# Optimization experiments

Hardware: AMD Instinct MI355X
Metric: run time of the kernel (lower is better)

## Reference

```python
import jax, jax.numpy as jnp
import numpy as np
from jax import lax

L1_DECAY = 1e-06


def _maxpool2(x):
    # NCHW 2x2 max pool, stride 2
    return lax.reduce_window(x, -jnp.inf, lax.max, (1, 1, 2, 2), (1, 1, 2, 2), 'VALID')


def _cnn(x, w1, b1, w2, b2, wo, bo):
    # x: [N,128,128] -> [N,64], z-score normalized over batch dim
    x = x[:, None]  # [N,1,128,128]
    dn = ('NCHW', 'OIHW', 'NCHW')
    x = lax.conv_general_dilated(x, w1, (1, 1), 'SAME', dimension_numbers=dn) + b1[None, :, None, None]
    x = _maxpool2(jax.nn.relu(x))  # [N,4,64,64]
    x = lax.conv_general_dilated(x, w2, (1, 1), 'SAME', dimension_numbers=dn) + b2[None, :, None, None]
    x = _maxpool2(jax.nn.relu(x))  # [N,8,32,32]
    x = x.reshape(x.shape[0], -1)  # [N,8192] (C,H,W order, as torch .view)
    x = x @ wo.T + bo  # [N,64]
    mean = x.mean(axis=0)
    std = x.std(axis=0, ddof=1)  # torch unbiased std
    return (x - mean) / std


def _interact(item, nbr):
    # item: [N,64]; nbr: [N,H,K,64]. dot-attention over K per node/hop.
    scores = jnp.einsum('nhkd,nd->nhk', nbr, item)
    attn = jax.nn.softmax(scores, axis=-1)
    return jnp.einsum('nhk,nhkd->nhd', attn, nbr)  # [N,H,64]


def setup_inputs() -> dict:
    key = jax.random.key(0)
    ks = jax.random.split(key, 16)
    B = 4096
    inp = {}
    inp['data'] = jax.random.randint(ks[0], (B, 3), 0, 76)
    inp['cell_nbr'] = jax.random.randint(ks[1], (76, 2, 128), 0, 15970)
    inp['drug_nbr'] = jax.random.randint(ks[2], (764, 2, 128), 0, 15970)
    inp['protein_table'] = jax.random.normal(ks[3], (15970, 64), jnp.float32)
    inp['cell_emb_pre'] = jax.random.normal(ks[4], (76, 128, 128), jnp.float32)
    inp['drug_emb_pre'] = jax.random.normal(ks[5], (764, 128, 128), jnp.float32)
    inp['conv1_w'] = 0.05 * jax.random.normal(ks[6], (4, 1, 3, 3), jnp.float32)
    inp['conv1_b'] = 0.05 * jax.random.normal(ks[7], (4,), jnp.float32)
    inp['conv2_w'] = 0.05 * jax.random.normal(ks[8], (8, 4, 3, 3), jnp.float32)
    inp['conv2_b'] = 0.05 * jax.random.normal(ks[9], (8,), jnp.float32)
    inp['out_w'] = 0.05 * jax.random.normal(ks[10], (64, 8192), jnp.float32)
    inp['out_b'] = 0.05 * jax.random.normal(ks[11], (64,), jnp.float32)
    inp['agg_w'] = 0.05 * jax.random.normal(ks[12], (64, 128), jnp.float32)
    inp['agg_b'] = 0.05 * jax.random.normal(ks[13], (64,), jnp.float32)
    inp['comb_w'] = 0.05 * jax.random.normal(ks[14], (64, 128), jnp.float32)
    return inp


def reference(data, cell_nbr, drug_nbr, protein_table, cell_emb_pre, drug_emb_pre,
              conv1_w, conv1_b, conv2_w, conv2_b, out_w, out_b, agg_w, agg_b, comb_w):
    cells, drug1, drug2 = data[:, 0], data[:, 1], data[:, 2]
    B = data.shape[0]

    # per-node neighbor embedding gather: [num, n_hop, K, 64]
    cell_nbr_emb = protein_table[cell_nbr]
    drug_nbr_emb = protein_table[drug_nbr]

    # CNN item embeddings from precomputed images
    cell_item = _cnn(cell_emb_pre, conv1_w, conv1_b, conv2_w, conv2_b, out_w, out_b)  # [76,64]
    drug_item = _cnn(drug_emb_pre, conv1_w, conv1_b, conv2_w, conv2_b, out_w, out_b)  # [764,64]

    # gather -> attend -> weighted sum, then concat hops and aggregate
    cell_i = _interact(cell_item, cell_nbr_emb).reshape(cell_item.shape[0], -1)  # [76,128]
    drug_i = _interact(drug_item, drug_nbr_emb).reshape(drug_item.shape[0], -1)  # [764,128]
    cell_emb = cell_i @ agg_w.T + agg_b  # [76,64]
    drug_emb = drug_i @ agg_w.T + agg_b  # [764,64]

    # batch gather, keep singleton dim 1 to match torch stacking of [1,64]
    ce = cell_emb[cells][:, None, :]   # [B,1,64]
    d1e = drug_emb[drug1][:, None, :]
    d2e = drug_emb[drug2][:, None, :]

    # therapy: transformation_matrix
    combined = jnp.concatenate([d1e, d2e], axis=2) @ comb_w.T  # [B,1,64]
    therapy = (combined * ce).sum(axis=2)  # [B,1]
    toxic = (d1e * d2e).sum(axis=2)        # [B,1]
    score = therapy - toxic

    # emb loss (faithful to source: neighbor lists are indexed on the BATCH dim by hop)
    cnl = cell_nbr_emb[cells]   # [B,2,128,64]
    dnl1 = drug_nbr_emb[drug1]
    dnl2 = drug_nbr_emb[drug2]
    sq = lambda t: jnp.sum(t * t)
    item_reg = (sq(ce) + sq(d1e) + sq(d2e)) / 2
    node_reg = jnp.float32(0.0)
    for hop in range(2):
        node_reg = node_reg + (sq(cnl[hop]) + sq(dnl1[hop]) + sq(dnl2[hop])) / 2
    emb_loss = L1_DECAY * (item_reg + node_reg) / B
    return score, emb_loss
```

## Files before the change

kernel.cpp:

```cpp
#include <hip/hip_runtime.h>
#include <hip/hip_bf16.h>
#include <math.h>

#define N_CELL 76
#define N_DRUG 764
#define N_ITEM 840
#define BATCH  4096

#define POOL2H_B 55050240u
#define POOL2L_B 68812800u
#define WHI_B    0u
#define WLO_B    1048576u
#define XFC_B    2097152u
#define ITEM_B   2312192u
#define EMB_B    2527232u
#define V_B      2742272u
#define LOSS_B   2781184u

typedef short bh8 __attribute__((ext_vector_type(8)));
typedef short bh4 __attribute__((ext_vector_type(4)));
typedef float f32x4 __attribute__((ext_vector_type(4)));

static __device__ inline unsigned short f2bf(float f) {
  union { float f; unsigned u; } v; v.f = f;
  unsigned r = v.u + 0x7FFFu + ((v.u >> 16) & 1u);
  return (unsigned short)(r >> 16);
}
static __device__ inline float bf2f(unsigned short h) {
  union { unsigned u; float f; } v; v.u = ((unsigned)h) << 16;
  return v.f;
}
static __device__ inline unsigned short f2bf_lo(float f, unsigned short h) {
  union { float f; unsigned u; } a; a.f = f - bf2f(h);
  return (unsigned short)(a.u >> 16);
}

__global__ __launch_bounds__(256) void k_conv1(
    const float* __restrict__ cell_pre, const float* __restrict__ drug_pre,
    const float* __restrict__ w1, const float* __restrict__ b1,
    float* __restrict__ pool1) {
  __shared__ float img[66 * 128];
  int half = blockIdx.x, n = blockIdx.y;
  int tid = threadIdx.x;
  int cy0 = half * 64;
  const float* src = (n < N_CELL) ? (cell_pre + (size_t)n * 16384)
                                  : (drug_pre + (size_t)(n - N_CELL) * 16384);
  for (int i = tid; i < 66 * 32; i += 256) {
    int r = i >> 5, c = i & 31;
    int iy = cy0 - 1 + r;
    float4 v = make_float4(0.f, 0.f, 0.f, 0.f);
    if (iy >= 0 && iy < 128) v = ((const float4*)src)[iy * 32 + c];
    ((float4*)img)[i] = v;
  }
  float wv[4][9], bb[4];
#pragma unroll
  for (int c = 0; c < 4; ++c) {
    bb[c] = b1[c];
#pragma unroll
    for (int j = 0; j < 9; ++j) wv[c][j] = w1[c * 9 + j];
  }
  __syncthreads();
  int t = tid & 31;
  int g = tid >> 5;
  const float4* img4 = (const float4*)img;
#pragma unroll 1
  for (int rpi = 0; rpi < 4; ++rpi) {
    int rp = g + 8 * rpi;
    int ly = 2 * rp;
    float4 rowv[4]; float lo[4], hi[4];
#pragma unroll
    for (int rr = 0; rr < 4; ++rr) {
      rowv[rr] = img4[(ly + rr) * 32 + t];
      float l = __shfl_up(rowv[rr].w, 1);
      float h = __shfl_down(rowv[rr].x, 1);
      lo[rr] = (t == 0) ? 0.f : l;
      hi[rr] = (t == 31) ? 0.f : h;
    }
    float a[2][4][4];
#pragma unroll
    for (int orow = 0; orow < 2; ++orow)
#pragma unroll
      for (int oc = 0; oc < 4; ++oc)
#pragma unroll
        for (int c = 0; c < 4; ++c) a[orow][oc][c] = bb[oc];
#pragma unroll
    for (int orow = 0; orow < 2; ++orow) {
#pragma unroll
      for (int kr = 0; kr < 3; ++kr) {
        int rr = orow + kr;
        float in[6] = {lo[rr], rowv[rr].x, rowv[rr].y, rowv[rr].z, rowv[rr].w, hi[rr]};
#pragma unroll
        for (int ks = 0; ks < 3; ++ks)
#pragma unroll
          for (int oc = 0; oc < 4; ++oc) {
            float w = wv[oc][kr * 3 + ks];
#pragma unroll
            for (int c = 0; c < 4; ++c) a[orow][oc][c] += in[c + ks] * w;
          }
      }
    }
#pragma unroll
    for (int pc = 0; pc < 2; ++pc) {
      float4 res;
      float* resf = (float*)&res;
#pragma unroll
      for (int oc = 0; oc < 4; ++oc) {
        float m = fmaxf(fmaxf(a[0][oc][2 * pc], a[0][oc][2 * pc + 1]),
                        fmaxf(a[1][oc][2 * pc], a[1][oc][2 * pc + 1]));
        resf[oc] = fmaxf(m, 0.f);
      }
      int py = half * 32 + rp, px = 2 * t + pc;
      ((float4*)pool1)[((size_t)n * 64 + py) * 64 + px] = res;
    }
  }
}

__global__ __launch_bounds__(256) void k_conv2(
    const float* __restrict__ pool1, const float* __restrict__ w2,
    const float* __restrict__ b2, unsigned short* __restrict__ pool2h,
    unsigned short* __restrict__ pool2l) {
  __shared__ unsigned short lh[34 * 66 * 4];
  __shared__ unsigned short ll[34 * 66 * 4];
  int half = blockIdx.x, n = blockIdx.y;
  int tid = threadIdx.x;
  int cy0 = half * 32;
  const float4* src = (const float4*)(pool1 + (size_t)n * 16384);
  for (int i = tid; i < 34 * 64; i += 256) {
    int r = i >> 6, c = i & 63;
    int iy = cy0 - 1 + r;
    float4 v = make_float4(0.f, 0.f, 0.f, 0.f);
    if (iy >= 0 && iy < 64) v = src[iy * 64 + c];
    ushort4 h, l;
    h.x = f2bf(v.x); l.x = f2bf_lo(v.x, h.x);
    h.y = f2bf(v.y); l.y = f2bf_lo(v.y, h.y);
    h.z = f2bf(v.z); l.z = f2bf_lo(v.z, h.z);
    h.w = f2bf(v.w); l.w = f2bf_lo(v.w, h.w);
    ((ushort4*)lh)[r * 66 + c + 1] = h;
    ((ushort4*)ll)[r * 66 + c + 1] = l;
  }
  if (tid < 68) {
    int r = tid >> 1, c = (tid & 1) ? 65 : 0;
    ushort4 z = make_ushort4(0, 0, 0, 0);
    ((ushort4*)lh)[r * 66 + c] = z;
    ((ushort4*)ll)[r * 66 + c] = z;
  }
  int wv_ = tid >> 6;
  int lane = tid & 63;
  int ml = lane & 15, q = lane >> 4;
  int oc_b = ml & 7, yv = ml >> 3;
  bh8 Bh[2], Bl[2];
#pragma unroll
  for (int ch = 0; ch < 2; ++ch) {
#pragma unroll
    for (int j = 0; j < 8; ++j) {
      int kg = ch * 32 + q * 8 + j;
      float v = 0.f;
      if (kg < 48) {
        int r = kg / 12, rem = kg - r * 12;
        int ks = rem >> 2, ic = rem & 3;
        int kr = r - yv;
        if (kr >= 0 && kr <= 2) v = w2[(oc_b * 4 + ic) * 9 + kr * 3 + ks];
      } else if (kg == 48) {
        v = b2[oc_b];
      }
      unsigned short h = f2bf(v);
      Bh[ch][j] = (short)h;
      Bl[ch][j] = (short)f2bf_lo(v, h);
    }
  }
  int c0 = 2 * q, c1 = 2 * q + 1;
  int c2 = 8 + 2 * q, c3 = 9 + 2 * q;
  if (c2 > 11) { c2 = 8; c3 = 9; }
  int r0 = (c0 * 86) >> 8, s0 = c0 - 3 * r0;
  int r1 = (c1 * 86) >> 8, s1 = c1 - 3 * r1;
  int r2 = (c2 * 86) >> 8, s2 = c2 - 3 * r2;
  int r3 = (c3 * 86) >> 8, s3 = c3 - 3 * r3;
  int x0 = (wv_ & 3) << 4;
  int off0 = r0 * 66 + x0 + ml + s0;
  int off1 = r1 * 66 + x0 + ml + s1;
  int off2 = r2 * 66 + x0 + ml + s2;
  int off3 = r3 * 66 + x0 + ml + s3;
  __syncthreads();
  const bh4* lh4 = (const bh4*)lh;
  const bh4* ll4 = (const bh4*)ll;
  union BH8U { bh8 v; struct { bh4 lo, hi; } s; };
#pragma unroll 1
  for (int rp = 0; rp < 16; ++rp) {
    int base = 2 * rp * 66;
    BH8U ah0, al0, ah1, al1;
    ah0.s.lo = lh4[base + off0]; ah0.s.hi = lh4[base + off1];
    al0.s.lo = ll4[base + off0]; al0.s.hi = ll4[base + off1];
    if (q < 2) {
      ah1.s.lo = lh4[base + off2]; ah1.s.hi = lh4[base + off3];
      al1.s.lo = ll4[base + off2]; al1.s.hi = ll4[base + off3];
    } else {
#pragma unroll
      for (int j = 0; j < 8; ++j) { ah1.v[j] = 0; al1.v[j] = 0; }
      if (q == 2) ah1.v[0] = (short)0x3F80;
    }
    f32x4 accA = {0.f, 0.f, 0.f, 0.f}, accB = accA;
    accA = __builtin_amdgcn_mfma_f32_16x16x32_bf16(ah0.v, Bh[0], accA, 0, 0, 0);
    accA = __builtin_amdgcn_mfma_f32_16x16x32_bf16(ah0.v, Bl[0], accA, 0, 0, 0);
    accA = __builtin_amdgcn_mfma_f32_16x16x32_bf16(al0.v, Bh[0], accA, 0, 0, 0);
    accB = __builtin_amdgcn_mfma_f32_16x16x32_bf16(ah1.v, Bh[1], accB, 0, 0, 0);
    accB = __builtin_amdgcn_mfma_f32_16x16x32_bf16(ah1.v, Bl[1], accB, 0, 0, 0);
    accB = __builtin_amdgcn_mfma_f32_16x16x32_bf16(al1.v, Bh[1], accB, 0, 0, 0);
    float d0 = accA[0] + accB[0], d1 = accA[1] + accB[1];
    float d2 = accA[2] + accB[2], d3 = accA[3] + accB[3];
    float m0 = fmaxf(d0, d1), m1 = fmaxf(d2, d3);
    float o0 = __shfl_xor(m0, 8), o1 = __shfl_xor(m1, 8);
    m0 = fmaxf(fmaxf(m0, o0), 0.f);
    m1 = fmaxf(fmaxf(m1, o1), 0.f);
    if (yv == 0) {
      unsigned short h0 = f2bf(m0), h1 = f2bf(m1);
      unsigned short l0 = f2bf(m0 - bf2f(h0)), l1 = f2bf(m1 - bf2f(h1));
      int PR = half * 16 + rp;
      unsigned ui = (unsigned)n * 4096u + (unsigned)oc_b * 512u +
                    (unsigned)PR * 16u + (unsigned)(x0 >> 2) + (unsigned)q;
      ((unsigned*)pool2h)[ui] = (unsigned)h0 | ((unsigned)h1 << 16);
      ((unsigned*)pool2l)[ui] = (unsigned)l0 | ((unsigned)l1 << 16);
    }
  }
}

__global__ __launch_bounds__(256) void k_cast(
    const float* __restrict__ out_w, unsigned short* __restrict__ whi,
    unsigned short* __restrict__ wlo, float* __restrict__ xfc,
    float* __restrict__ loss) {
  int gid = blockIdx.x * 256 + threadIdx.x;
  if (gid == 0) *loss = 0.f;
  float4 v = ((const float4*)out_w)[gid];
  ushort4 h, l;
  h.x = f2bf(v.x); l.x = f2bf(v.x - bf2f(h.x));
  h.y = f2bf(v.y); l.y = f2bf(v.y - bf2f(h.y));
  h.z = f2bf(v.z); l.z = f2bf(v.z - bf2f(h.z));
  h.w = f2bf(v.w); l.w = f2bf(v.w - bf2f(h.w));
  ((ushort4*)whi)[gid] = h;
  ((ushort4*)wlo)[gid] = l;
  if (gid < N_ITEM * 64) xfc[gid] = 0.f;
}

__global__ __launch_bounds__(64) void k_fc(
    const unsigned short* __restrict__ pool2h, const unsigned short* __restrict__ pool2l,
    const unsigned short* __restrict__ whi, const unsigned short* __restrict__ wlo,
    float* __restrict__ xfc) {
  int mt = blockIdx.x, kc = blockIdx.y;
  int lane = threadIdx.x;
  int ml = lane & 15, q = lane >> 4;
  int row = mt * 16 + ml; if (row > N_ITEM - 1) row = N_ITEM - 1;
  size_t k0 = (size_t)kc * 256 + q * 8;
  const bh8* Ah = (const bh8*)(pool2h + (size_t)row * 8192 + k0);
  const bh8* Al = (const bh8*)(pool2l + (size_t)row * 8192 + k0);
  const bh8* Bh[4], * Bl[4];
#pragma unroll
  for (int nb = 0; nb < 4; ++nb) {
    Bh[nb] = (const bh8*)(whi + (size_t)(nb * 16 + ml) * 8192 + k0);
    Bl[nb] = (const bh8*)(wlo + (size_t)(nb * 16 + ml) * 8192 + k0);
  }
  f32x4 acc[4];
#pragma unroll
  for (int nb = 0; nb < 4; ++nb) acc[nb] = (f32x4){0.f, 0.f, 0.f, 0.f};
#pragma unroll
  for (int st = 0; st < 8; ++st) {
    bh8 ah = Ah[st * 4], al = Al[st * 4];
#pragma unroll
    for (int nb = 0; nb < 4; ++nb) {
      bh8 bhv = Bh[nb][st * 4], blv = Bl[nb][st * 4];
      acc[nb] = __builtin_amdgcn_mfma_f32_16x16x32_bf16(ah, bhv, acc[nb], 0, 0, 0);
      acc[nb] = __builtin_amdgcn_mfma_f32_16x16x32_bf16(ah, blv, acc[nb], 0, 0, 0);
      acc[nb] = __builtin_amdgcn_mfma_f32_16x16x32_bf16(al, bhv, acc[nb], 0, 0, 0);
    }
  }
#pragma unroll
  for (int r = 0; r < 4; ++r) {
    int mr = mt * 16 + q * 4 + r;
    if (mr < N_ITEM) {
      float* dst = xfc + (size_t)mr * 64 + ml;
#pragma unroll
      for (int nb = 0; nb < 4; ++nb) atomicAdd(dst + nb * 16, acc[nb][r]);
    }
  }
}

__global__ __launch_bounds__(256) void k_norm(
    const float* __restrict__ xfc, float* __restrict__ item) {
  __shared__ float red[256];
  int grp = blockIdx.x >> 6;
  int o = blockIdx.x & 63;
  int base = grp ? N_CELL : 0;
  int N = grp ? N_DRUG : N_CELL;
  int tid = threadIdx.x;
  float s = 0.f;
  for (int i = tid; i < N; i += 256) s += xfc[(size_t)(base + i) * 64 + o];
  red[tid] = s; __syncthreads();
  for (int w = 128; w > 0; w >>= 1) { if (tid < w) red[tid] += red[tid + w]; __syncthreads(); }
  float mean = red[0] / (float)N;
  __syncthreads();
  float sq = 0.f;
  for (int i = tid; i < N; i += 256) {
    float d = xfc[(size_t)(base + i) * 64 + o] - mean;
    sq += d * d;
  }
  red[tid] = sq; __syncthreads();
  for (int w = 128; w > 0; w >>= 1) { if (tid < w) red[tid] += red[tid + w]; __syncthreads(); }
  float inv_std = 1.f / sqrtf(red[0] / (float)(N - 1));
  for (int i = tid; i < N; i += 256)
    item[(size_t)(base + i) * 64 + o] = (xfc[(size_t)(base + i) * 64 + o] - mean) * inv_std;
}

__global__ __launch_bounds__(256) void k_interact(
    const int* __restrict__ cell_nbr, const int* __restrict__ drug_nbr,
    const float* __restrict__ protein, const float* __restrict__ item,
    const float* __restrict__ agg_w, const float* __restrict__ agg_b,
    float* __restrict__ emb) {
  __shared__ float pb[128 * 65];
  __shared__ float item_s[64];
  __shared__ float sc[128];
  __shared__ float hop_out[128];
  __shared__ float red[256];
  int n = blockIdx.x;
  int tid = threadIdx.x;
  const int* nbr = (n < N_CELL) ? (cell_nbr + (size_t)n * 256)
                                : (drug_nbr + (size_t)(n - N_CELL) * 256);
  if (tid < 64) item_s[tid] = item[(size_t)n * 64 + tid];
  __syncthreads();
  for (int h = 0; h < 2; ++h) {
    for (int e = tid; e < 8192; e += 256) {
      int k = e >> 6, d = e & 63;
      int idx = nbr[h * 128 + k];
      pb[k * 65 + d] = protein[(size_t)idx * 64 + d];
    }
    __syncthreads();
    {
      int k = tid >> 1, halfd = tid & 1;
      int d0 = halfd * 32;
      float p = 0.f;
#pragma unroll
      for (int d = 0; d < 32; ++d) p += item_s[d0 + d] * pb[k * 65 + d0 + d];
      p += __shfl_xor(p, 1);
      if (halfd == 0) sc[k] = p;
    }
    __syncthreads();
    if (tid < 64) {
      float a = sc[tid], b = sc[tid + 64];
      float m = fmaxf(a, b);
#pragma unroll
      for (int off = 32; off > 0; off >>= 1) m = fmaxf(m, __shfl_xor(m, off));
      float e0 = __expf(a - m), e1 = __expf(b - m);
      float s = e0 + e1;
#pragma unroll
      for (int off = 32; off > 0; off >>= 1) s += __shfl_xor(s, off);
      float inv = 1.f / s;
      sc[tid] = e0 * inv; sc[tid + 64] = e1 * inv;
    }
    __syncthreads();
    {
      int d = tid & 63, kq = tid >> 6;
      float p = 0.f;
#pragma unroll
      for (int k = 0; k < 32; ++k) {
        int kk = kq * 32 + k;
        p += sc[kk] * pb[kk * 65 + d];
      }
      red[tid] = p;
    }
    __syncthreads();
    if (tid < 64)
      hop_out[h * 64 + tid] = red[tid] + red[tid + 64] + red[tid + 128] + red[tid + 192];
    __syncthreads();
  }
  {
    int o = tid & 63, jq = tid >> 6;
    float p = 0.f;
#pragma unroll
    for (int j = 0; j < 32; ++j) {
      int jj = jq * 32 + j;
      p += hop_out[jj] * agg_w[(size_t)o * 128 + jj];
    }
    red[tid] = p;
  }
  __syncthreads();
  if (tid < 64)
    emb[(size_t)n * 64 + tid] =
        red[tid] + red[tid + 64] + red[tid + 128] + red[tid + 192] + agg_b[tid];
}

__global__ __launch_bounds__(128) void k_cellv(
    const float* __restrict__ emb, const float* __restrict__ comb_w,
    float* __restrict__ V) {
  __shared__ float ce[64];
  int c = blockIdx.x;
  int j = threadIdx.x;
  if (j < 64) ce[j] = emb[(size_t)c * 64 + j];
  __syncthreads();
  float s = 0.f;
#pragma unroll
  for (int o = 0; o < 64; ++o) s += comb_w[(size_t)o * 128 + j] * ce[o];
  V[(size_t)c * 128 + j] = s;
}

__global__ __launch_bounds__(256) void k_score(
    const int* __restrict__ data, const float* __restrict__ emb,
    const float* __restrict__ V, float* __restrict__ out,
    float* __restrict__ loss) {
  __shared__ float racc[4];
  int tid = threadIdx.x;
  int lane = tid & 63;
  int w = tid >> 6;
  int b = blockIdx.x * 4 + w;
  int c = data[b * 3 + 0], d1 = data[b * 3 + 1], d2 = data[b * 3 + 2];
  float ce = emb[(size_t)c * 64 + lane];
  float e1 = emb[(size_t)(N_CELL + d1) * 64 + lane];
  float e2 = emb[(size_t)(N_CELL + d2) * 64 + lane];
  float v1 = V[(size_t)c * 128 + lane];
  float v2 = V[(size_t)c * 128 + 64 + lane];
  float th = e1 * v1 + e2 * v2;
  float tx = e1 * e2;
  float rg = ce * ce + e1 * e1 + e2 * e2;
#pragma unroll
  for (int off = 32; off > 0; off >>= 1) {
    th += __shfl_xor(th, off);
    tx += __shfl_xor(tx, off);
    rg += __shfl_xor(rg, off);
  }
  if (lane == 0) { out[b] = th - tx; racc[w] = rg; }
  __syncthreads();
  if (tid == 0) atomicAdd(loss, 0.5f * (racc[0] + racc[1] + racc[2] + racc[3]));
}

__global__ __launch_bounds__(256) void k_nodereg(
    const int* __restrict__ data, const int* __restrict__ cell_nbr,
    const int* __restrict__ drug_nbr, const float* __restrict__ protein,
    float* __restrict__ loss) {
  __shared__ float red[256];
  int j = blockIdx.x;
  int hop = j / 3, which = j % 3;
  int row = data[hop * 3 + which];
  const int* nbr = (which == 0) ? (cell_nbr + (size_t)row * 256)
                                : (drug_nbr + (size_t)row * 256);
  int tid = threadIdx.x;
  float acc = 0.f;
  for (int e = tid; e < 16384; e += 256) {
    int k = e >> 6, d = e & 63;
    float v = protein[(size_t)nbr[k] * 64 + d];
    acc += v * v;
  }
  red[tid] = acc; __syncthreads();
  for (int w = 128; w > 0; w >>= 1) { if (tid < w) red[tid] += red[tid + w]; __syncthreads(); }
  if (tid == 0) atomicAdd(loss, 0.5f * red[0]);
}

__global__ void k_finalize(const float* __restrict__ loss, float* __restrict__ out) {
  if (threadIdx.x == 0) out[BATCH] = loss[0] * (1e-6f / 4096.f);
}

extern "C" void kernel_launch(void* const* d_in, const int* in_sizes, int n_in,
                              void* d_out, int out_size, void* d_ws, size_t ws_size,
                              hipStream_t stream) {
  const int*   data      = (const int*)d_in[0];
  const int*   cell_nbr  = (const int*)d_in[1];
  const int*   drug_nbr  = (const int*)d_in[2];
  const float* protein   = (const float*)d_in[3];
  const float* cell_pre  = (const float*)d_in[4];
  const float* drug_pre  = (const float*)d_in[5];
  const float* w1        = (const float*)d_in[6];
  const float* b1        = (const float*)d_in[7];
  const float* w2        = (const float*)d_in[8];
  const float* b2        = (const float*)d_in[9];
  const float* out_w     = (const float*)d_in[10];
  const float* agg_w     = (const float*)d_in[12];
  const float* agg_b     = (const float*)d_in[13];
  const float* comb_w    = (const float*)d_in[14];
  float* out = (float*)d_out;
  char* base = (char*)d_ws;
  float* pool1            = (float*)base;
  unsigned short* pool2h  = (unsigned short*)(base + POOL2H_B);
  unsigned short* pool2l  = (unsigned short*)(base + POOL2L_B);
  unsigned short* whi     = (unsigned short*)(base + WHI_B);
  unsigned short* wlo     = (unsigned short*)(base + WLO_B);
  float* xfc              = (float*)(base + XFC_B);
  float* item             = (float*)(base + ITEM_B);
  float* emb              = (float*)(base + EMB_B);
  float* V                = (float*)(base + V_B);
  float* loss             = (float*)(base + LOSS_B);

  k_conv1<<<dim3(2, 840), 256, 0, stream>>>(cell_pre, drug_pre, w1, b1, pool1);
  k_conv2<<<dim3(2, 840), 256, 0, stream>>>(pool1, w2, b2, pool2h, pool2l);
  k_cast<<<512, 256, 0, stream>>>(out_w, whi, wlo, xfc, loss);
  k_fc<<<dim3(53, 32), 64, 0, stream>>>(pool2h, pool2l, whi, wlo, xfc);
  k_norm<<<128, 256, 0, stream>>>(xfc, item);
  k_interact<<<840, 256, 0, stream>>>(cell_nbr, drug_nbr, protein, item, agg_w, agg_b, emb);
  k_cellv<<<N_CELL, 128, 0, stream>>>(emb, comb_w, V);
  k_score<<<1024, 256, 0, stream>>>(data, emb, V, out, loss);
  k_nodereg<<<6, 256, 0, stream>>>(data, cell_nbr, drug_nbr, protein, loss);
  k_finalize<<<1, 64, 0, stream>>>(loss, out);
}
```

Before: 256.3 us.

## Compute conv1 with split-bf16 MFMA instead of scalar FMAs

Rewrites the first convolution kernel to stage the input tile in shared memory as high/low bf16 pairs and compute the 3x3 conv as 16x16x32 MFMA matrix ops, three products per output to approximate fp32. Max-pooling is done with lane shuffles and the bias and ReLU are applied after pooling. It targets the scalar FMA cost of conv1 but adds conversion work, doubled shared-memory traffic and scattered scalar stores to pool1 in place of float4 stores. Precision is slightly below full fp32.

```diff
diff --git a/kernel.cpp b/kernel.cpp
--- a/kernel.cpp
+++ b/kernel.cpp
@@ -35,82 +35,96 @@
   return (unsigned short)(a.u >> 16);
 }
 
+union BH8U { bh8 v; struct { bh4 lo, hi; } s; };
+
 __global__ __launch_bounds__(256) void k_conv1(
     const float* __restrict__ cell_pre, const float* __restrict__ drug_pre,
     const float* __restrict__ w1, const float* __restrict__ b1,
     float* __restrict__ pool1) {
-  __shared__ float img[66 * 128];
+  __shared__ unsigned short lh[66 * 34 * 4];
+  __shared__ unsigned short ll[66 * 34 * 4];
   int half = blockIdx.x, n = blockIdx.y;
   int tid = threadIdx.x;
   int cy0 = half * 64;
-  const float* src = (n < N_CELL) ? (cell_pre + (size_t)n * 16384)
-                                  : (drug_pre + (size_t)(n - N_CELL) * 16384);
+  const float4* src = (const float4*)((n < N_CELL) ? (cell_pre + (size_t)n * 16384)
+                                                   : (drug_pre + (size_t)(n - N_CELL) * 16384));
   for (int i = tid; i < 66 * 32; i += 256) {
-    int r = i >> 5, c = i & 31;
-    int iy = cy0 - 1 + r;
+    int lr = i >> 5, g = i & 31;
+    int iy = cy0 - 1 + lr;
     float4 v = make_float4(0.f, 0.f, 0.f, 0.f);
-    if (iy >= 0 && iy < 128) v = ((const float4*)src)[iy * 32 + c];
-    ((float4*)img)[i] = v;
-  }
-  float wv[4][9], bb[4];
-#pragma unroll
-  for (int c = 0; c < 4; ++c) {
-    bb[c] = b1[c];
-#pragma unroll
-    for (int j = 0; j < 9; ++j) wv[c][j] = w1[c * 9 + j];
-  }
-  __syncthreads();
-  int t = tid & 31;
-  int g = tid >> 5;
-  const float4* img4 = (const float4*)img;
+    if (iy >= 0 && iy < 128) v = src[iy * 32 + g];
+    ushort4 h, l;
+    h.x = f2bf(v.x); l.x = f2bf_lo(v.x, h.x);
+    h.y = f2bf(v.y); l.y = f2bf_lo(v.y, h.y);
+    h.z = f2bf(v.z); l.z = f2bf_lo(v.z, h.z);
+    h.w = f2bf(v.w); l.w = f2bf_lo(v.w, h.w);
+    ((ushort4*)lh)[lr * 34 + g + 1] = h;
+    ((ushort4*)ll)[lr * 34 + g + 1] = l;
+  }
+  if (tid < 132) {
+    int lr = tid >> 1, g = (tid & 1) ? 33 : 0;
+    ushort4 z = make_ushort4(0, 0, 0, 0);
+    ((ushort4*)lh)[lr * 34 + g] = z;
+    ((ushort4*)ll)[lr * 34 + g] = z;
+  }
+  int wv_ = tid >> 6;
+  int lane = tid & 63;
+  int ml = lane & 15, q = lane >> 4;
+  int oc = ml & 3, yv = (ml >> 2) & 1, hi = ml >> 3;
+  float bb = b1[oc];
+  bh8 BhE, BlE, BhO, BlO;
+  {
+    int kr = q - yv;
+    bool krok = (kr >= 0 && kr <= 2);
+#pragma unroll
+    for (int j = 0; j < 8; ++j) {
+      float ve = 0.f, vo = 0.f;
+      if (krok) {
+        int kse = j - 3 - 2 * hi;
+        int kso = j - 2 * hi;
+        if (kse >= 0 && kse <= 2) ve = w1[oc * 9 + kr * 3 + kse];
+        if (kso >= 0 && kso <= 2) vo = w1[oc * 9 + kr * 3 + kso];
+      }
+      unsigned short he = f2bf(ve), ho = f2bf(vo);
+      BhE[j] = (short)he; BlE[j] = (short)f2bf_lo(ve, he);
+      BhO[j] = (short)ho; BlO[j] = (short)f2bf_lo(vo, ho);
+    }
+  }
+  __syncthreads();
+  int x0 = (wv_ & 1) * 16;
+  int rp0 = (wv_ >> 1) * 16;
+  int Lb = x0 + ml;
+  const bh4* lh4 = (const bh4*)lh;
+  const bh4* ll4 = (const bh4*)ll;
 #pragma unroll 1
-  for (int rpi = 0; rpi < 4; ++rpi) {
-    int rp = g + 8 * rpi;
-    int ly = 2 * rp;
-    float4 rowv[4]; float lo[4], hi[4];
-#pragma unroll
-    for (int rr = 0; rr < 4; ++rr) {
-      rowv[rr] = img4[(ly + rr) * 32 + t];
-      float l = __shfl_up(rowv[rr].w, 1);
-      float h = __shfl_down(rowv[rr].x, 1);
-      lo[rr] = (t == 0) ? 0.f : l;
-      hi[rr] = (t == 31) ? 0.f : h;
-    }
-    float a[2][4][4];
-#pragma unroll
-    for (int orow = 0; orow < 2; ++orow)
-#pragma unroll
-      for (int oc = 0; oc < 4; ++oc)
-#pragma unroll
-        for (int c = 0; c < 4; ++c) a[orow][oc][c] = bb[oc];
-#pragma unroll
-    for (int orow = 0; orow < 2; ++orow) {
-#pragma unroll
-      for (int kr = 0; kr < 3; ++kr) {
-        int rr = orow + kr;
-        float in[6] = {lo[rr], rowv[rr].x, rowv[rr].y, rowv[rr].z, rowv[rr].w, hi[rr]};
-#pragma unroll
-        for (int ks = 0; ks < 3; ++ks)
-#pragma unroll
-          for (int oc = 0; oc < 4; ++oc) {
-            float w = wv[oc][kr * 3 + ks];
-#pragma unroll
-            for (int c = 0; c < 4; ++c) a[orow][oc][c] += in[c + ks] * w;
-          }
+  for (int i = 0; i < 16; ++i) {
+    int rp = rp0 + i;
+    int lr = 2 * rp + q;
+    int base = lr * 34 + Lb;
+    bh4 g0h = lh4[base], g1h = lh4[base + 1], g2h = lh4[base + 2];
+    bh4 g0l = ll4[base], g1l = ll4[base + 1], g2l = ll4[base + 2];
+    BH8U aeh, ael, aoh, aol;
+    aeh.s.lo = g0h; aeh.s.hi = g1h;
+    ael.s.lo = g0l; ael.s.hi = g1l;
+    aoh.s.lo = g1h; aoh.s.hi = g2h;
+    aol.s.lo = g1l; aol.s.hi = g2l;
+    f32x4 de = {0.f, 0.f, 0.f, 0.f}, dd = de;
+    de = __builtin_amdgcn_mfma_f32_16x16x32_bf16(aeh.v, BhE, de, 0, 0, 0);
+    de = __builtin_amdgcn_mfma_f32_16x16x32_bf16(aeh.v, BlE, de, 0, 0, 0);
+    de = __builtin_amdgcn_mfma_f32_16x16x32_bf16(ael.v, BhE, de, 0, 0, 0);
+    dd = __builtin_amdgcn_mfma_f32_16x16x32_bf16(aoh.v, BhO, dd, 0, 0, 0);
+    dd = __builtin_amdgcn_mfma_f32_16x16x32_bf16(aoh.v, BlO, dd, 0, 0, 0);
+    dd = __builtin_amdgcn_mfma_f32_16x16x32_bf16(aol.v, BhO, dd, 0, 0, 0);
+    int py = half * 32 + rp;
+#pragma unroll
+    for (int r = 0; r < 4; ++r) {
+      float t = fmaxf(de[r], dd[r]);
+      float t2 = __shfl_xor(t, 4);
+      if (yv == 0) {
+        float val = fmaxf(fmaxf(t, t2) + bb, 0.f);
+        int px = 2 * (x0 + q * 4 + r) + hi;
+        pool1[(((size_t)n * 64 + py) * 64 + px) * 4 + oc] = val;
       }
-    }
-#pragma unroll
-    for (int pc = 0; pc < 2; ++pc) {
-      float4 res;
-      float* resf = (float*)&res;
-#pragma unroll
-      for (int oc = 0; oc < 4; ++oc) {
-        float m = fmaxf(fmaxf(a[0][oc][2 * pc], a[0][oc][2 * pc + 1]),
-                        fmaxf(a[1][oc][2 * pc], a[1][oc][2 * pc + 1]));
-        resf[oc] = fmaxf(m, 0.f);
-      }
-      int py = half * 32 + rp, px = 2 * t + pc;
-      ((float4*)pool1)[((size_t)n * 64 + py) * 64 + px] = res;
     }
   }
 }
@@ -183,7 +197,6 @@
   __syncthreads();
   const bh4* lh4 = (const bh4*)lh;
   const bh4* ll4 = (const bh4*)ll;
-  union BH8U { bh8 v; struct { bh4 lo, hi; } s; };
 #pragma unroll 1
   for (int rp = 0; rp < 16; ++rp) {
     int base = 2 * rp * 66;
```

After: 257.1 us. Within noise of the previous version (+0.3%).
